# Kernel optimization log

Hardware: AMD Instinct MI355X
Metric: run time of the kernel (lower is better)

Reference implementation:

```python
import jax, jax.numpy as jnp
import numpy as np

EPS = 1e-6

def _l2norm(x):
    # torch F.normalize(dim=1): x / max(||x||_2, eps), norm over channel axis 1
    n = jnp.sqrt(jnp.sum(x * x, axis=1, keepdims=True))
    return x / jnp.maximum(n, EPS)

def setup_inputs() -> dict:
    key = jax.random.key(0)
    ks = jax.random.split(key, 8)
    B, C, Cenc, dk, dv, H, W = 2, 320, 326, 64, 64, 64, 64
    return {
        "x": jax.random.normal(ks[0], (B, C, H, W), jnp.float32),
        "x_enc": jax.random.normal(ks[1], (B, Cenc, H, W), jnp.float32),
        "Wq": jax.random.normal(ks[2], (dk, Cenc), jnp.float32) * 0.05,
        "bq": jnp.zeros((dk,), jnp.float32),
        "Wk": jax.random.normal(ks[3], (dk, Cenc), jnp.float32) * 0.05,
        "bk": jnp.zeros((dk,), jnp.float32),
        "Wv": jax.random.normal(ks[4], (dv, C), jnp.float32) * 0.05,
        "bv": jnp.zeros((dv,), jnp.float32),
    }

def reference(x, x_enc, Wq, bq, Wk, bk, Wv, bv):
    B, C, H, Wd = x.shape
    L = H * Wd
    xe = x_enc.reshape(B, x_enc.shape[1], L)   # [B, Cenc, L]
    xf = x.reshape(B, C, L)                    # [B, C, L]
    # 1x1 conv projections == channel matmuls
    Q = jnp.einsum('oc,bcl->bol', Wq, xe) + bq[None, :, None]  # [B, dk, L]
    K = jnp.einsum('oc,bcl->bol', Wk, xe) + bk[None, :, None]  # [B, dk, L]
    V = jnp.einsum('oc,bcl->bol', Wv, xf) + bv[None, :, None]  # [B, dv, L]
    # cosine (L2-normalized) attention
    Qn = _l2norm(Q)
    Kn = _l2norm(K)
    A = jax.nn.softmax(jnp.einsum('bqi,bqj->bij', Qn, Kn), axis=-1)  # [B, L, L]
    R = jnp.einsum('bij,bvj->bvi', A, V)       # [B, dv, L]
    return R.reshape(B, V.shape[1], H, Wd)
```

## Files before the change

kernel.cpp:

```cpp
#include <hip/hip_runtime.h>


#define L_DIM 4096
#define KPAD 384
#define NSPLIT 8

typedef __attribute__((ext_vector_type(8))) short bf16x8;
typedef __attribute__((ext_vector_type(4))) float f32x4;

__device__ __forceinline__ unsigned short f2bf(float f) {
    unsigned u = __float_as_uint(f);
    u += 0x7fffu + ((u >> 16) & 1u);
    return (unsigned short)(u >> 16);
}

__global__ __launch_bounds__(256) void wconv_kernel(
    const float* __restrict__ Wq, const float* __restrict__ Wk,
    const float* __restrict__ Wv, unsigned short* __restrict__ wbf)
{
    const int idx = blockIdx.x * 256 + threadIdx.x;
    if (idx >= 3 * 64 * KPAD) return;
    const int t = idx / (64 * KPAD);
    const int rem = idx - t * 64 * KPAD;
    const int d = rem / KPAD, c = rem - d * KPAD;
    const int Cin = (t == 2) ? 320 : 326;
    const float* W = (t == 0) ? Wq : (t == 1 ? Wk : Wv);
    wbf[idx] = (c < Cin) ? f2bf(W[(size_t)d * Cin + c]) : (unsigned short)0;
}

__global__ __launch_bounds__(256) void xpose_kernel(
    const float* __restrict__ x, const float* __restrict__ xe,
    unsigned short* __restrict__ xt_x, unsigned short* __restrict__ xt_xe)
{
    const int z = blockIdx.z;
    const int src_is_x = z >> 1, b = z & 1;
    const int c0 = blockIdx.y * 64;
    const int l0 = blockIdx.x * 64;
    const int Cin = src_is_x ? 320 : 326;
    const float* src = (src_is_x ? x : xe) + (size_t)b * Cin * L_DIM;
    unsigned short* dst = (src_is_x ? xt_x : xt_xe) + (size_t)b * L_DIM * KPAD;

    __shared__ float tile[64][65];
    const int tid = threadIdx.x;

    for (int it = 0; it < 16; ++it) {
        const int idx = tid + it * 256;
        const int cc = idx >> 6, ll = idx & 63;
        const int c = c0 + cc;
        tile[cc][ll] = (c < Cin) ? src[(size_t)c * L_DIM + l0 + ll] : 0.f;
    }
    __syncthreads();
    for (int it = 0; it < 4; ++it) {
        const int idx = tid + it * 256;
        const int ll = idx >> 4, cq = idx & 15;
        ushort4 o;
        o.x = f2bf(tile[cq * 4 + 0][ll]);
        o.y = f2bf(tile[cq * 4 + 1][ll]);
        o.z = f2bf(tile[cq * 4 + 2][ll]);
        o.w = f2bf(tile[cq * 4 + 3][ll]);
        *(ushort4*)(dst + (size_t)(l0 + ll) * KPAD + c0 + cq * 4) = o;
    }
}

__global__ __launch_bounds__(64) void proj_kernel(
    const unsigned short* __restrict__ xt_xe, const unsigned short* __restrict__ xt_x,
    const unsigned short* __restrict__ wbf,
    const float* __restrict__ bq, const float* __restrict__ bk,
    const float* __restrict__ bv,
    unsigned short* __restrict__ qn, unsigned short* __restrict__ kn,
    unsigned short* __restrict__ vbf)
{
    const int z = blockIdx.y;
    const int tensor = z >> 1, b = z & 1;
    const int l0 = blockIdx.x * 64;
    const int lane = threadIdx.x;
    const int q = lane >> 4, ln = lane & 15;

    const unsigned short* Xt = (tensor == 2 ? xt_x : xt_xe) + (size_t)b * L_DIM * KPAD;
    const unsigned short* W  = wbf + (size_t)tensor * 64 * KPAD;
    const float* bias = (tensor == 0) ? bq : (tensor == 1 ? bk : bv);
    const int ksteps = (tensor == 2) ? 10 : 11;

    f32x4 acc[4][4];
    #pragma unroll
    for (int mf = 0; mf < 4; ++mf)
        #pragma unroll
        for (int nf = 0; nf < 4; ++nf) acc[mf][nf] = (f32x4){0.f, 0.f, 0.f, 0.f};

    bf16x8 af[4], bfr[4], afn[4], bfn[4];
    #pragma unroll
    for (int mf = 0; mf < 4; ++mf)
        af[mf] = *(const bf16x8*)(W + (size_t)(mf * 16 + ln) * KPAD + q * 8);
    #pragma unroll
    for (int nf = 0; nf < 4; ++nf)
        bfr[nf] = *(const bf16x8*)(Xt + (size_t)(l0 + nf * 16 + ln) * KPAD + q * 8);

    for (int ks = 0; ks < ksteps; ++ks) {
        if (ks + 1 < ksteps) {
            const int c = (ks + 1) * 32 + q * 8;
            #pragma unroll
            for (int mf = 0; mf < 4; ++mf)
                afn[mf] = *(const bf16x8*)(W + (size_t)(mf * 16 + ln) * KPAD + c);
            #pragma unroll
            for (int nf = 0; nf < 4; ++nf)
                bfn[nf] = *(const bf16x8*)(Xt + (size_t)(l0 + nf * 16 + ln) * KPAD + c);
        }
        #pragma unroll
        for (int mf = 0; mf < 4; ++mf)
            #pragma unroll
            for (int nf = 0; nf < 4; ++nf)
                acc[mf][nf] = __builtin_amdgcn_mfma_f32_16x16x32_bf16(
                    af[mf], bfr[nf], acc[mf][nf], 0, 0, 0);
        #pragma unroll
        for (int mf = 0; mf < 4; ++mf) af[mf] = afn[mf];
        #pragma unroll
        for (int nf = 0; nf < 4; ++nf) bfr[nf] = bfn[nf];
    }

    #pragma unroll
    for (int mf = 0; mf < 4; ++mf)
        #pragma unroll
        for (int r = 0; r < 4; ++r) {
            const float bb = bias[mf * 16 + q * 4 + r];
            #pragma unroll
            for (int nf = 0; nf < 4; ++nf) acc[mf][nf][r] += bb;
        }

    if (tensor < 2) {
        unsigned short* outp = (tensor ? kn : qn) + (size_t)b * L_DIM * 64;
        #pragma unroll
        for (int nf = 0; nf < 4; ++nf) {
            float s = 0.f;
            #pragma unroll
            for (int mf = 0; mf < 4; ++mf)
                #pragma unroll
                for (int r = 0; r < 4; ++r) s += acc[mf][nf][r] * acc[mf][nf][r];
            s += __shfl_xor(s, 16);
            s += __shfl_xor(s, 32);
            const float rn = 1.0f / fmaxf(sqrtf(s), 1e-6f);
            const size_t lrow = (size_t)(l0 + nf * 16 + ln) * 64;
            #pragma unroll
            for (int mf = 0; mf < 4; ++mf) {
                ushort4 o;
                o.x = f2bf(acc[mf][nf][0] * rn);
                o.y = f2bf(acc[mf][nf][1] * rn);
                o.z = f2bf(acc[mf][nf][2] * rn);
                o.w = f2bf(acc[mf][nf][3] * rn);
                *(ushort4*)(outp + lrow + mf * 16 + q * 4) = o;
            }
        }
    } else {
        unsigned short* outp = vbf + (size_t)b * 64 * L_DIM;
        #pragma unroll
        for (int mf = 0; mf < 4; ++mf)
            #pragma unroll
            for (int r = 0; r < 4; ++r) {
                const int v = mf * 16 + q * 4 + r;
                #pragma unroll
                for (int nf = 0; nf < 4; ++nf)
                    outp[(size_t)v * L_DIM + l0 + nf * 16 + ln] = f2bf(acc[mf][nf][r]);
            }
    }
}

__global__ __launch_bounds__(256) void attn_kernel(
    const unsigned short* __restrict__ qn, const unsigned short* __restrict__ kn,
    const unsigned short* __restrict__ vbf,
    float* __restrict__ opart, float* __restrict__ ssum)
{
    const int b = blockIdx.z, split = blockIdx.y;
    const int i0 = blockIdx.x * 128;
    const int tid = threadIdx.x;
    const int w = tid >> 6, lane = tid & 63, q = lane >> 4, ln = lane & 15;

    const unsigned short* Q = qn + (size_t)b * L_DIM * 64;
    const unsigned short* K = kn + (size_t)b * L_DIM * 64;
    const unsigned short* V = vbf + (size_t)b * 64 * L_DIM;

    __shared__ unsigned short Kb[64][72];
    __shared__ unsigned short Vb[64][72];
    __shared__ unsigned short Pl[4][32][72];

    bf16x8 qa[2][2];
    #pragma unroll
    for (int s = 0; s < 2; ++s) {
        const unsigned short* qp = Q + (size_t)(i0 + w * 32 + s * 16 + ln) * 64 + q * 8;
        qa[s][0] = *(const bf16x8*)(qp);
        qa[s][1] = *(const bf16x8*)(qp + 32);
    }

    f32x4 acc[2][4];
    #pragma unroll
    for (int s = 0; s < 2; ++s)
        #pragma unroll
        for (int vf = 0; vf < 4; ++vf) acc[s][vf] = (f32x4){0.f, 0.f, 0.f, 0.f};
    float rowsum[2][4] = {{0.f,0.f,0.f,0.f},{0.f,0.f,0.f,0.f}};
    const f32x4 zero = (f32x4){0.f, 0.f, 0.f, 0.f};

    const int jbase = split * (L_DIM / NSPLIT);
    const int JT = L_DIM / (NSPLIT * 64);

    bf16x8 kst[2], vst[2];
    #pragma unroll
    for (int p = 0; p < 2; ++p) {
        const int idx = p * 256 + tid;
        kst[p] = *(const bf16x8*)(K + (size_t)jbase * 64 + idx * 8);
        vst[p] = *(const bf16x8*)(V + (size_t)(idx >> 3) * L_DIM + jbase + (idx & 7) * 8);
    }
    #pragma unroll
    for (int p = 0; p < 2; ++p) {
        const int idx = p * 256 + tid;
        *(bf16x8*)&Kb[idx >> 3][(idx & 7) * 8] = kst[p];
        *(bf16x8*)&Vb[idx >> 3][(idx & 7) * 8] = vst[p];
    }
    __syncthreads();

    for (int jt = 0; jt < JT; ++jt) {
        if (jt + 1 < JT) {
            const int j0 = jbase + (jt + 1) * 64;
            #pragma unroll
            for (int p = 0; p < 2; ++p) {
                const int idx = p * 256 + tid;
                kst[p] = *(const bf16x8*)(K + (size_t)j0 * 64 + idx * 8);
                vst[p] = *(const bf16x8*)(V + (size_t)(idx >> 3) * L_DIM + j0 + (idx & 7) * 8);
            }
        }

        bf16x8 kf[4][2];
        #pragma unroll
        for (int jf = 0; jf < 4; ++jf) {
            kf[jf][0] = *(const bf16x8*)&Kb[jf * 16 + ln][q * 8];
            kf[jf][1] = *(const bf16x8*)&Kb[jf * 16 + ln][q * 8 + 32];
        }

        #pragma unroll
        for (int s = 0; s < 2; ++s) {
            f32x4 sv[4];
            #pragma unroll
            for (int jf = 0; jf < 4; ++jf) {
                sv[jf] = __builtin_amdgcn_mfma_f32_16x16x32_bf16(qa[s][0], kf[jf][0], zero, 0, 0, 0);
                sv[jf] = __builtin_amdgcn_mfma_f32_16x16x32_bf16(qa[s][1], kf[jf][1], sv[jf], 0, 0, 0);
            }
            #pragma unroll
            for (int jf = 0; jf < 4; ++jf)
                #pragma unroll
                for (int r = 0; r < 4; ++r) {
                    const float p = __expf(sv[jf][r]);
                    rowsum[s][r] += p;
                    Pl[w][s * 16 + q * 4 + r][jf * 16 + ln] = f2bf(p);
                }
        }

        bf16x8 vfr[4][2];
        #pragma unroll
        for (int vf = 0; vf < 4; ++vf) {
            vfr[vf][0] = *(const bf16x8*)&Vb[vf * 16 + ln][q * 8];
            vfr[vf][1] = *(const bf16x8*)&Vb[vf * 16 + ln][q * 8 + 32];
        }

        #pragma unroll
        for (int s = 0; s < 2; ++s) {
            const bf16x8 pa0 = *(const bf16x8*)&Pl[w][s * 16 + ln][q * 8];
            const bf16x8 pa1 = *(const bf16x8*)&Pl[w][s * 16 + ln][q * 8 + 32];
            #pragma unroll
            for (int vf = 0; vf < 4; ++vf) {
                acc[s][vf] = __builtin_amdgcn_mfma_f32_16x16x32_bf16(pa0, vfr[vf][0], acc[s][vf], 0, 0, 0);
                acc[s][vf] = __builtin_amdgcn_mfma_f32_16x16x32_bf16(pa1, vfr[vf][1], acc[s][vf], 0, 0, 0);
            }
        }

        __syncthreads();
        if (jt + 1 < JT) {
            #pragma unroll
            for (int p = 0; p < 2; ++p) {
                const int idx = p * 256 + tid;
                *(bf16x8*)&Kb[idx >> 3][(idx & 7) * 8] = kst[p];
                *(bf16x8*)&Vb[idx >> 3][(idx & 7) * 8] = vst[p];
            }
            __syncthreads();
        }
    }

    #pragma unroll
    for (int off = 1; off < 16; off <<= 1)
        #pragma unroll
        for (int s = 0; s < 2; ++s)
            #pragma unroll
            for (int r = 0; r < 4; ++r)
                rowsum[s][r] += __shfl_xor(rowsum[s][r], off);

    float* Op = opart + ((size_t)(b * NSPLIT + split) * L_DIM + i0 + w * 32) * 64;
    #pragma unroll
    for (int s = 0; s < 2; ++s)
        #pragma unroll
        for (int vf = 0; vf < 4; ++vf)
            #pragma unroll
            for (int r = 0; r < 4; ++r)
                Op[(s * 16 + q * 4 + r) * 64 + vf * 16 + ln] = acc[s][vf][r];

    if (ln == 0) {
        #pragma unroll
        for (int s = 0; s < 2; ++s)
            #pragma unroll
            for (int r = 0; r < 4; ++r)
                ssum[(size_t)(b * NSPLIT + split) * L_DIM + i0 + w * 32 + s * 16 + q * 4 + r]
                    = rowsum[s][r];
    }
}

__global__ __launch_bounds__(256) void combine_kernel(
    const float* __restrict__ opart, const float* __restrict__ ssum,
    float* __restrict__ out)
{
    const int b = blockIdx.y;
    const int i0 = blockIdx.x * 64;
    const int tid = threadIdx.x;
    __shared__ float t[64][65];
    __shared__ float sinv[64];

    if (tid < 64) {
        float s = 0.f;
        for (int sp = 0; sp < NSPLIT; ++sp)
            s += ssum[(size_t)(b * NSPLIT + sp) * L_DIM + i0 + tid];
        sinv[tid] = 1.0f / s;
    }
    __syncthreads();
    for (int idx = tid; idx < 4096; idx += 256) {
        const int i = idx >> 6, v = idx & 63;
        float a = 0.f;
        for (int sp = 0; sp < NSPLIT; ++sp)
            a += opart[((size_t)(b * NSPLIT + sp) * L_DIM + i0 + i) * 64 + v];
        t[i][v] = a;
    }
    __syncthreads();
    for (int idx = tid; idx < 4096; idx += 256) {
        const int v = idx >> 6, i = idx & 63;
        out[((size_t)(b * 64 + v)) * L_DIM + i0 + i] = t[i][v] * sinv[i];
    }
}

extern "C" void kernel_launch(void* const* d_in, const int* in_sizes, int n_in,
                              void* d_out, int out_size, void* d_ws, size_t ws_size,
                              hipStream_t stream)
{
    const float* x  = (const float*)d_in[0];
    const float* xe = (const float*)d_in[1];
    const float* Wq = (const float*)d_in[2];
    const float* bq = (const float*)d_in[3];
    const float* Wk = (const float*)d_in[4];
    const float* bk = (const float*)d_in[5];
    const float* Wv = (const float*)d_in[6];
    const float* bv = (const float*)d_in[7];
    float* out = (float*)d_out;

    char* ws = (char*)d_ws;
    unsigned short* qn   = (unsigned short*)(ws);
    unsigned short* kn   = (unsigned short*)(ws + (1u << 20));
    unsigned short* vbf  = (unsigned short*)(ws + (2u << 20));
    float*          ss   = (float*)(ws + (3u << 20));
    unsigned short* wb   = (unsigned short*)(ws + (3u << 20) + (512u << 10));
    unsigned short* xtxe = (unsigned short*)(ws + (4u << 20));
    unsigned short* xtx  = (unsigned short*)(ws + (10u << 20));
    float*          op   = (float*)(ws + (8u << 20));

    wconv_kernel<<<dim3((3 * 64 * KPAD + 255) / 256), 256, 0, stream>>>(Wq, Wk, Wv, wb);
    xpose_kernel<<<dim3(64, 6, 4), 256, 0, stream>>>(x, xe, xtx, xtxe);
    proj_kernel<<<dim3(64, 6), 64, 0, stream>>>(xtxe, xtx, wb, bq, bk, bv, qn, kn, vbf);
    attn_kernel<<<dim3(32, NSPLIT, 2), 256, 0, stream>>>(qn, kn, vbf, op, ss);
    combine_kernel<<<dim3(64, 2), 256, 0, stream>>>(op, ss, out);
}
```

Before: 131.5 us.

## Transpose MFMA operands so score tiles store row-contiguous and merge prep kernels

The attention kernel swaps the A/B operands of both MFMAs so that each lane holds four consecutive key columns of one query row. This lets probabilities be written to LDS as packed 4-wide stores, collapses the row-sum into one scalar per tile with two cross-lane shuffles, and turns the partial-output writes into float4 stores. Separately, the weight-conversion and transpose kernels are merged into a single launch using an extra grid z-slice, saving one kernel launch. The operand swap changes the register layout of the accumulators, so indexing in the epilogue must match exactly.

```diff
diff --git a/kernel.cpp b/kernel.cpp
--- a/kernel.cpp
+++ b/kernel.cpp
@@ -14,25 +14,27 @@
     return (unsigned short)(u >> 16);
 }
 
-__global__ __launch_bounds__(256) void wconv_kernel(
+__global__ __launch_bounds__(256) void prep_kernel(
+    const float* __restrict__ x, const float* __restrict__ xe,
     const float* __restrict__ Wq, const float* __restrict__ Wk,
-    const float* __restrict__ Wv, unsigned short* __restrict__ wbf)
-{
-    const int idx = blockIdx.x * 256 + threadIdx.x;
-    if (idx >= 3 * 64 * KPAD) return;
-    const int t = idx / (64 * KPAD);
-    const int rem = idx - t * 64 * KPAD;
-    const int d = rem / KPAD, c = rem - d * KPAD;
-    const int Cin = (t == 2) ? 320 : 326;
-    const float* W = (t == 0) ? Wq : (t == 1 ? Wk : Wv);
-    wbf[idx] = (c < Cin) ? f2bf(W[(size_t)d * Cin + c]) : (unsigned short)0;
-}
-
-__global__ __launch_bounds__(256) void xpose_kernel(
-    const float* __restrict__ x, const float* __restrict__ xe,
-    unsigned short* __restrict__ xt_x, unsigned short* __restrict__ xt_xe)
+    const float* __restrict__ Wv,
+    unsigned short* __restrict__ xt_x, unsigned short* __restrict__ xt_xe,
+    unsigned short* __restrict__ wbf)
 {
     const int z = blockIdx.z;
+    if (z == 4) {
+        const int bid = blockIdx.y * 64 + blockIdx.x;
+        const int idx = bid * 256 + threadIdx.x;
+        if (idx >= 3 * 64 * KPAD) return;
+        const int t = idx / (64 * KPAD);
+        const int rem = idx - t * 64 * KPAD;
+        const int d = rem / KPAD, c = rem - d * KPAD;
+        const int Cin = (t == 2) ? 320 : 326;
+        const float* W = (t == 0) ? Wq : (t == 1 ? Wk : Wv);
+        wbf[idx] = (c < Cin) ? f2bf(W[(size_t)d * Cin + c]) : (unsigned short)0;
+        return;
+    }
+
     const int src_is_x = z >> 1, b = z & 1;
     const int c0 = blockIdx.y * 64;
     const int l0 = blockIdx.x * 64;
@@ -194,7 +196,7 @@
     for (int s = 0; s < 2; ++s)
         #pragma unroll
         for (int vf = 0; vf < 4; ++vf) acc[s][vf] = (f32x4){0.f, 0.f, 0.f, 0.f};
-    float rowsum[2][4] = {{0.f,0.f,0.f,0.f},{0.f,0.f,0.f,0.f}};
+    float rowsum[2] = {0.f, 0.f};
     const f32x4 zero = (f32x4){0.f, 0.f, 0.f, 0.f};
 
     const int jbase = split * (L_DIM / NSPLIT);
@@ -235,20 +237,20 @@
 
         #pragma unroll
         for (int s = 0; s < 2; ++s) {
-            f32x4 sv[4];
             #pragma unroll
             for (int jf = 0; jf < 4; ++jf) {
-                sv[jf] = __builtin_amdgcn_mfma_f32_16x16x32_bf16(qa[s][0], kf[jf][0], zero, 0, 0, 0);
-                sv[jf] = __builtin_amdgcn_mfma_f32_16x16x32_bf16(qa[s][1], kf[jf][1], sv[jf], 0, 0, 0);
-            }
-            #pragma unroll
-            for (int jf = 0; jf < 4; ++jf)
-                #pragma unroll
-                for (int r = 0; r < 4; ++r) {
-                    const float p = __expf(sv[jf][r]);
-                    rowsum[s][r] += p;
-                    Pl[w][s * 16 + q * 4 + r][jf * 16 + ln] = f2bf(p);
-                }
+                f32x4 st;
+                st = __builtin_amdgcn_mfma_f32_16x16x32_bf16(kf[jf][0], qa[s][0], zero, 0, 0, 0);
+                st = __builtin_amdgcn_mfma_f32_16x16x32_bf16(kf[jf][1], qa[s][1], st, 0, 0, 0);
+                const float p0 = __expf(st[0]);
+                const float p1 = __expf(st[1]);
+                const float p2 = __expf(st[2]);
+                const float p3 = __expf(st[3]);
+                rowsum[s] += (p0 + p1) + (p2 + p3);
+                ushort4 pk;
+                pk.x = f2bf(p0); pk.y = f2bf(p1); pk.z = f2bf(p2); pk.w = f2bf(p3);
+                *(ushort4*)&Pl[w][s * 16 + ln][jf * 16 + q * 4] = pk;
+            }
         }
 
         bf16x8 vfr[4][2];
@@ -260,12 +262,12 @@
 
         #pragma unroll
         for (int s = 0; s < 2; ++s) {
-            const bf16x8 pa0 = *(const bf16x8*)&Pl[w][s * 16 + ln][q * 8];
-            const bf16x8 pa1 = *(const bf16x8*)&Pl[w][s * 16 + ln][q * 8 + 32];
+            const bf16x8 pb0 = *(const bf16x8*)&Pl[w][s * 16 + ln][q * 8];
+            const bf16x8 pb1 = *(const bf16x8*)&Pl[w][s * 16 + ln][q * 8 + 32];
             #pragma unroll
             for (int vf = 0; vf < 4; ++vf) {
-                acc[s][vf] = __builtin_amdgcn_mfma_f32_16x16x32_bf16(pa0, vfr[vf][0], acc[s][vf], 0, 0, 0);
-                acc[s][vf] = __builtin_amdgcn_mfma_f32_16x16x32_bf16(pa1, vfr[vf][1], acc[s][vf], 0, 0, 0);
+                acc[s][vf] = __builtin_amdgcn_mfma_f32_16x16x32_bf16(vfr[vf][0], pb0, acc[s][vf], 0, 0, 0);
+                acc[s][vf] = __builtin_amdgcn_mfma_f32_16x16x32_bf16(vfr[vf][1], pb1, acc[s][vf], 0, 0, 0);
             }
         }
 
@@ -282,29 +284,27 @@
     }
 
     #pragma unroll
-    for (int off = 1; off < 16; off <<= 1)
+    for (int s = 0; s < 2; ++s) {
+        rowsum[s] += __shfl_xor(rowsum[s], 16);
+        rowsum[s] += __shfl_xor(rowsum[s], 32);
+    }
+
+    float* Op = opart + ((size_t)(b * NSPLIT + split) * L_DIM + i0 + w * 32) * 64;
+    #pragma unroll
+    for (int s = 0; s < 2; ++s)
+        #pragma unroll
+        for (int vf = 0; vf < 4; ++vf) {
+            float4 o;
+            o.x = acc[s][vf][0]; o.y = acc[s][vf][1];
+            o.z = acc[s][vf][2]; o.w = acc[s][vf][3];
+            *(float4*)&Op[(s * 16 + ln) * 64 + vf * 16 + q * 4] = o;
+        }
+
+    if (q == 0) {
         #pragma unroll
         for (int s = 0; s < 2; ++s)
-            #pragma unroll
-            for (int r = 0; r < 4; ++r)
-                rowsum[s][r] += __shfl_xor(rowsum[s][r], off);
-
-    float* Op = opart + ((size_t)(b * NSPLIT + split) * L_DIM + i0 + w * 32) * 64;
-    #pragma unroll
-    for (int s = 0; s < 2; ++s)
-        #pragma unroll
-        for (int vf = 0; vf < 4; ++vf)
-            #pragma unroll
-            for (int r = 0; r < 4; ++r)
-                Op[(s * 16 + q * 4 + r) * 64 + vf * 16 + ln] = acc[s][vf][r];
-
-    if (ln == 0) {
-        #pragma unroll
-        for (int s = 0; s < 2; ++s)
-            #pragma unroll
-            for (int r = 0; r < 4; ++r)
-                ssum[(size_t)(b * NSPLIT + split) * L_DIM + i0 + w * 32 + s * 16 + q * 4 + r]
-                    = rowsum[s][r];
+            ssum[(size_t)(b * NSPLIT + split) * L_DIM + i0 + w * 32 + s * 16 + ln]
+                = rowsum[s];
     }
 }
 
@@ -363,8 +363,7 @@
     unsigned short* xtx  = (unsigned short*)(ws + (10u << 20));
     float*          op   = (float*)(ws + (8u << 20));
 
-    wconv_kernel<<<dim3((3 * 64 * KPAD + 255) / 256), 256, 0, stream>>>(Wq, Wk, Wv, wb);
-    xpose_kernel<<<dim3(64, 6, 4), 256, 0, stream>>>(x, xe, xtx, xtxe);
+    prep_kernel<<<dim3(64, 6, 5), 256, 0, stream>>>(x, xe, Wq, Wk, Wv, xtx, xtxe, wb);
     proj_kernel<<<dim3(64, 6), 64, 0, stream>>>(xtxe, xtx, wb, bq, bk, bv, qn, kn, vbf);
     attn_kernel<<<dim3(32, NSPLIT, 2), 256, 0, stream>>>(qn, kn, vbf, op, ss);
     combine_kernel<<<dim3(64, 2), 256, 0, stream>>>(op, ss, out);
```

Result: faster. 128.4 us (-2.4%).
